# Kernel optimization log

Measured on AMD Instinct MI355X. Metric: run time of the kernel, lower is better.

## Reference

```python
import math
import jax, jax.numpy as jnp
import numpy as np

D_MODEL = 1024
NHEAD = 16
DK = D_MODEL // NHEAD
FACTOR = 5
B, L = 4, 8192
U = max(1, min(FACTOR * math.ceil(math.log(L + 1)), L))  # 50


def setup_inputs() -> dict:
    key = jax.random.key(0)
    ks = jax.random.split(key, 10)
    s = 1.0 / math.sqrt(D_MODEL)
    inp = {
        "x": jax.random.normal(ks[0], (B, L, D_MODEL), dtype=jnp.float32),
        "Wq": jax.random.normal(ks[1], (D_MODEL, D_MODEL), dtype=jnp.float32) * s,
        "bq": jnp.zeros((D_MODEL,), dtype=jnp.float32),
        "Wk": jax.random.normal(ks[2], (D_MODEL, D_MODEL), dtype=jnp.float32) * s,
        "bk": jnp.zeros((D_MODEL,), dtype=jnp.float32),
        "Wv": jax.random.normal(ks[3], (D_MODEL, D_MODEL), dtype=jnp.float32) * s,
        "bv": jnp.zeros((D_MODEL,), dtype=jnp.float32),
        "Wo": jax.random.normal(ks[4], (D_MODEL, D_MODEL), dtype=jnp.float32) * s,
        "bo": jnp.zeros((D_MODEL,), dtype=jnp.float32),
        # randperm(L)[:U] sample of key positions (constant, like torch.randperm)
        "idx_k": jax.random.permutation(ks[5], L)[:U].astype(jnp.int32),
    }
    return inp


def reference(x, Wq, bq, Wk, bk, Wv, bv, Wo, bo, idx_k):
    Bv, Lv, _ = x.shape
    H, dk = NHEAD, DK
    u = idx_k.shape[0]
    scale = 1.0 / math.sqrt(dk)

    # projections -> [B, H, L, dk]
    Q = (x @ Wq.T + bq).reshape(Bv, Lv, H, dk).transpose(0, 2, 1, 3)
    K = (x @ Wk.T + bk).reshape(Bv, Lv, H, dk).transpose(0, 2, 1, 3)
    V = (x @ Wv.T + bv).reshape(Bv, Lv, H, dk).transpose(0, 2, 1, 3)

    # sampled scores against u random keys: [B, H, L, u]
    K_samp = K[:, :, idx_k, :]
    scores = jnp.einsum("bhld,bhud->bhlu", Q, K_samp) * scale
    M = scores.max(-1) - scores.mean(-1)                 # [B, H, L]
    _, top_idx = jax.lax.top_k(M, u)                      # [B, H, u]

    # gather selected queries and attend against ALL keys
    Q_top = jnp.take_along_axis(Q, top_idx[..., None], axis=2)   # [B, H, u, dk]
    attn = jax.nn.softmax(jnp.einsum("bhud,bhld->bhul", Q_top, K) * scale, axis=-1)
    ctx_top = jnp.einsum("bhul,bhld->bhud", attn, V)              # [B, H, u, dk]

    # mean(V) fallback, scatter selected contexts back
    ctx = jnp.broadcast_to(V.mean(axis=2, keepdims=True), (Bv, H, Lv, dk))
    bidx = jnp.arange(Bv)[:, None, None]
    hidx = jnp.arange(H)[None, :, None]
    ctx = ctx.at[bidx, hidx, top_idx].set(ctx_top)

    ctx = ctx.transpose(0, 2, 1, 3).reshape(Bv, Lv, H * dk)
    return ctx @ Wo.T + bo
```

## Files before the change

### kernel.cpp

```cpp
#include <hip/hip_runtime.h>
#include <hip/hip_bf16.h>

#define B_ 4
#define L_ 8192
#define D_ 1024
#define H_ 16
#define SCALE 0.125f
#define NC 8
#define QPAD 64
#define RS 72

typedef __attribute__((ext_vector_type(8))) short bf16x8;
typedef __attribute__((ext_vector_type(4))) float f32x4;

__device__ __forceinline__ void gl2lds16(const void* g, void* s) {
    __builtin_amdgcn_global_load_lds(
        (const __attribute__((address_space(1))) unsigned int*)g,
        (__attribute__((address_space(3))) unsigned int*)s, 16, 0, 0);
}

__device__ __forceinline__ unsigned short bfbits(float a) {
    __hip_bfloat16 h = __float2bfloat16(a);
    return *(unsigned short*)&h;
}
__device__ __forceinline__ float bf2f(unsigned short u) {
    return __uint_as_float(((unsigned)u) << 16);
}

__global__ __launch_bounds__(256) void split3_kernel(const float* __restrict__ in,
        unsigned short* __restrict__ ph, unsigned short* __restrict__ pm,
        unsigned short* __restrict__ pl, int n4) {
    int i = blockIdx.x * 256 + threadIdx.x;
    if (i >= n4) return;
    float4 v = ((const float4*)in)[i];
    float c[4] = {v.x, v.y, v.z, v.w};
    unsigned short h[4], m[4], l[4];
    #pragma unroll
    for (int j = 0; j < 4; ++j) {
        float a = c[j];
        unsigned short hb = bfbits(a);
        float rh = a - bf2f(hb);
        unsigned short mb = bfbits(rh);
        float rm = rh - bf2f(mb);
        h[j] = hb; m[j] = mb; l[j] = bfbits(rm);
    }
    ((ushort4*)ph)[i] = *(ushort4*)h;
    ((ushort4*)pm)[i] = *(ushort4*)m;
    ((ushort4*)pl)[i] = *(ushort4*)l;
}

__global__ __launch_bounds__(256) void split2_kernel(const float* __restrict__ in,
        unsigned short* __restrict__ ph, unsigned short* __restrict__ pm, int n4) {
    int i = blockIdx.x * 256 + threadIdx.x;
    if (i >= n4) return;
    float4 v = ((const float4*)in)[i];
    float c[4] = {v.x, v.y, v.z, v.w};
    unsigned short h[4], m[4];
    #pragma unroll
    for (int j = 0; j < 4; ++j) {
        float a = c[j];
        unsigned short hb = bfbits(a);
        float rh = a - bf2f(hb);
        h[j] = hb; m[j] = bfbits(rh);
    }
    ((ushort4*)ph)[i] = *(ushort4*)h;
    ((ushort4*)pm)[i] = *(ushort4*)m;
}

__global__ __launch_bounds__(256) void xmean_kernel(const float* __restrict__ x,
                                                    float* __restrict__ xmean) {
    int c = blockIdx.x;
    int j = blockIdx.y * 256 + threadIdx.x;
    int b = blockIdx.z;
    const float* xp = x + ((size_t)b * L_ + (size_t)c * 256) * D_ + j;
    float s = 0.f;
    for (int l = 0; l < 256; ++l) s += xp[(size_t)l * D_];
    atomicAdd(&xmean[b * D_ + j], s * (1.0f / L_));
}

__global__ __launch_bounds__(256) void vecmat_kernel(const float* __restrict__ in,
                                                     const float* __restrict__ W,
                                                     const float* __restrict__ bias,
                                                     float* __restrict__ out) {
    __shared__ float vs[D_];
    int b = blockIdx.y;
    int j = blockIdx.x * 256 + threadIdx.x;
    for (int t = threadIdx.x; t < D_; t += 256) vs[t] = in[b * D_ + t];
    __syncthreads();
    const float* wr = W + (size_t)j * D_;
    float acc = 0.f;
    #pragma unroll 4
    for (int k = 0; k < D_; k += 4) {
        float4 w4 = *(const float4*)(wr + k);
        acc += vs[k] * w4.x + vs[k + 1] * w4.y + vs[k + 2] * w4.z + vs[k + 3] * w4.w;
    }
    out[b * D_ + j] = acc + bias[j];
}

__global__ __launch_bounds__(256) void ksamp_kernel(const float* __restrict__ x,
                                                    const float* __restrict__ Wk,
                                                    const float* __restrict__ bk,
                                                    const int* __restrict__ idx_k,
                                                    float* __restrict__ Ksamp, int U) {
    __shared__ float vs[D_];
    int u = blockIdx.x, b = blockIdx.y;
    int row = idx_k[u];
    const float* xp = x + ((size_t)b * L_ + row) * D_;
    for (int t = threadIdx.x; t < D_; t += 256) vs[t] = xp[t];
    __syncthreads();
    #pragma unroll
    for (int r = 0; r < 4; ++r) {
        int j = r * 256 + threadIdx.x;
        const float* wr = Wk + (size_t)j * D_;
        float acc = 0.f;
        #pragma unroll 4
        for (int k = 0; k < D_; k += 4) {
            float4 w4 = *(const float4*)(wr + k);
            acc += vs[k] * w4.x + vs[k + 1] * w4.y + vs[k + 2] * w4.z + vs[k + 3] * w4.w;
        }
        Ksamp[((size_t)b * U + u) * D_ + j] = acc + bk[j];
    }
}

#define TM 128
#define TN 128
#define BK 32
#define TSZ (TM * BK)

__global__ __launch_bounds__(256) void qkv_mfma(
    const unsigned short* __restrict__ xh, const unsigned short* __restrict__ xm,
    const unsigned short* __restrict__ xl,
    const unsigned short* __restrict__ qh, const unsigned short* __restrict__ qm,
    const unsigned short* __restrict__ ql,
    const unsigned short* __restrict__ kh, const unsigned short* __restrict__ km,
    const unsigned short* __restrict__ vh, const unsigned short* __restrict__ vm,
    const float* __restrict__ bq, const float* __restrict__ bk2, const float* __restrict__ bv,
    float* __restrict__ Q, __hip_bfloat16* __restrict__ Kb, __hip_bfloat16* __restrict__ Vb) {
    __shared__ __align__(16) unsigned short As[3][TSZ];
    __shared__ __align__(16) unsigned short Bs[3][TSZ];

    const int f    = blockIdx.y * 24 + blockIdx.x;
    const int w    = (f & 7) * 768 + (f >> 3);
    const int mblk = w / 24;
    const int nblk = w - mblk * 24;
    const int m0   = mblk * TM;
    const int n0   = nblk * TN;
    const int tid  = threadIdx.x;

    const float* bias; int which; int nb;
    if (n0 < 1024)      { which = 0; nb = n0;        bias = bq;  }
    else if (n0 < 2048) { which = 1; nb = n0 - 1024; bias = bk2; }
    else                { which = 2; nb = n0 - 2048; bias = bv;  }

    const int srow = tid >> 2;
    const int scol = (tid & 3) * 8;

    const int wave = tid >> 6;
    const int lane = tid & 63;
    const int wm = (wave & 1) * 64;
    const int wn = (wave >> 1) * 64;
    const int fr = lane & 15;
    const int fk = (lane >> 4) * 8;
    const int rbase = (lane >> 4) * 4;

    f32x4 acc[4][4];
    #pragma unroll
    for (int i = 0; i < 4; ++i)
        #pragma unroll
        for (int j = 0; j < 4; ++j)
            acc[i][j] = (f32x4){0.f, 0.f, 0.f, 0.f};

    const size_t aBase = (size_t)(m0 + srow) * D_ + scol;
    const size_t bBase = (size_t)(nb + srow) * D_ + scol;

    bf16x8 af[4], bfv[4];
    auto loadA = [&](const unsigned short* t) {
        #pragma unroll
        for (int i = 0; i < 4; ++i)
            af[i] = *(const bf16x8*)(t + (wm + i * 16 + fr) * BK + fk);
    };
    auto loadB = [&](const unsigned short* t) {
        #pragma unroll
        for (int j = 0; j < 4; ++j)
            bfv[j] = *(const bf16x8*)(t + (wn + j * 16 + fr) * BK + fk);
    };
    auto prod = [&]() {
        #pragma unroll
        for (int i = 0; i < 4; ++i)
            #pragma unroll
            for (int j = 0; j < 4; ++j)
                acc[i][j] = __builtin_amdgcn_mfma_f32_16x16x32_bf16(
                    af[i], bfv[j], acc[i][j], 0, 0, 0);
    };
    auto stage = [&](const unsigned short* g, unsigned short* s, int kt, size_t base) {
        gl2lds16(g + base + kt, s + tid * 8);
        gl2lds16(g + base + (size_t)64 * D_ + kt, s + tid * 8 + 2048);
    };

    if (which == 0) {
        for (int kt = 0; kt < D_; kt += BK) {
            stage(xh, &As[0][0], kt, aBase);
            stage(xm, &As[1][0], kt, aBase);
            stage(xl, &As[2][0], kt, aBase);
            stage(qh, &Bs[0][0], kt, bBase);
            stage(qm, &Bs[1][0], kt, bBase);
            stage(ql, &Bs[2][0], kt, bBase);
            __syncthreads();
            loadA(&As[0][0]); loadB(&Bs[0][0]); prod();
            loadB(&Bs[1][0]); prod();
            loadB(&Bs[2][0]); prod();
            loadA(&As[1][0]); loadB(&Bs[0][0]); prod();
            loadB(&Bs[1][0]); prod();
            loadA(&As[2][0]); loadB(&Bs[0][0]); prod();
            __syncthreads();
        }
    } else {
        const unsigned short* Bh = (which == 1) ? kh : vh;
        const unsigned short* Bm = (which == 1) ? km : vm;
        for (int kt = 0; kt < D_; kt += BK) {
            stage(xh, &As[0][0], kt, aBase);
            stage(xm, &As[1][0], kt, aBase);
            stage(Bh, &Bs[0][0], kt, bBase);
            stage(Bm, &Bs[1][0], kt, bBase);
            __syncthreads();
            loadA(&As[0][0]); loadB(&Bs[0][0]); prod();
            loadB(&Bs[1][0]); prod();
            loadA(&As[1][0]); loadB(&Bs[0][0]); prod();
            __syncthreads();
        }
    }

    float biasv[4];
    #pragma unroll
    for (int j = 0; j < 4; ++j) biasv[j] = bias[nb + wn + j * 16 + fr];

    #pragma unroll
    for (int i = 0; i < 4; ++i) {
        #pragma unroll
        for (int r = 0; r < 4; ++r) {
            size_t row = (size_t)(m0 + wm + i * 16 + rbase + r);
            #pragma unroll
            for (int j = 0; j < 4; ++j) {
                float v = acc[i][j][r] + biasv[j];
                int n = nb + wn + j * 16 + fr;
                if (which == 0)      Q[row * D_ + n] = v;
                else if (which == 1) Kb[row * D_ + n] = __float2bfloat16(v);
                else                 Vb[row * D_ + n] = __float2bfloat16(v);
            }
        }
    }
}

__global__ __launch_bounds__(256) void m_kernel(const float* __restrict__ Q,
                                                const float* __restrict__ Ksamp,
                                                float* __restrict__ M, int U) {
    __shared__ float ks[64 * 64];
    int lc = blockIdx.x, h = blockIdx.y, b = blockIdx.z;
    for (int t = threadIdx.x; t < U * 64; t += 256) {
        int u = t >> 6, d = t & 63;
        ks[t] = Ksamp[((size_t)b * U + u) * D_ + h * 64 + d];
    }
    __syncthreads();
    int l = lc * 256 + threadIdx.x;
    const float* qp = Q + ((size_t)b * L_ + l) * D_ + h * 64;
    float q[64];
    #pragma unroll
    for (int i = 0; i < 16; ++i) *(float4*)&q[i * 4] = *(const float4*)(qp + i * 4);
    float mx = -INFINITY, sm = 0.f;
    for (int u = 0; u < U; ++u) {
        const float* kp = &ks[u * 64];
        float dot = 0.f;
        #pragma unroll
        for (int d = 0; d < 64; ++d) dot = fmaf(q[d], kp[d], dot);
        dot *= SCALE;
        mx = fmaxf(mx, dot);
        sm += dot;
    }
    M[((size_t)(b * H_ + h)) * L_ + l] = mx - sm / (float)U;
}

__global__ __launch_bounds__(256) void topk_kernel(const float* __restrict__ M,
                                                   int* __restrict__ topidx, int U) {
    __shared__ float vals[L_];
    __shared__ float wv[4];
    __shared__ int   wi[4];
    __shared__ int   sbest;
    int bh = blockIdx.x;
    const float* mp = M + (size_t)bh * L_;
    for (int t = threadIdx.x; t < L_; t += 256) vals[t] = mp[t];
    __syncthreads();

    float bv = -INFINITY; int bi = 0x7fffffff;
    for (int t = threadIdx.x; t < L_; t += 256) {
        float v = vals[t];
        if (v > bv || (v == bv && t < bi)) { bv = v; bi = t; }
    }
    const int lane = threadIdx.x & 63, wave = threadIdx.x >> 6;

    for (int u = 0; u < U; ++u) {
        float rv = bv; int ri = bi;
        #pragma unroll
        for (int s = 1; s < 64; s <<= 1) {
            float v2 = __shfl_xor(rv, s, 64);
            int   i2 = __shfl_xor(ri, s, 64);
            if (v2 > rv || (v2 == rv && i2 < ri)) { rv = v2; ri = i2; }
        }
        if (lane == 0) { wv[wave] = rv; wi[wave] = ri; }
        __syncthreads();
        if (threadIdx.x == 0) {
            float fv = wv[0]; int fi = wi[0];
            #pragma unroll
            for (int w = 1; w < 4; ++w) {
                if (wv[w] > fv || (wv[w] == fv && wi[w] < fi)) { fv = wv[w]; fi = wi[w]; }
            }
            topidx[bh * U + u] = fi;
            sbest = fi;
            vals[fi] = -INFINITY;
        }
        __syncthreads();
        int fi = sbest;
        if ((fi & 255) == threadIdx.x) {
            bv = -INFINITY; bi = 0x7fffffff;
            for (int t = threadIdx.x; t < L_; t += 256) {
                float v = vals[t];
                if (v > bv || (v == bv && t < bi)) { bv = v; bi = t; }
            }
        }
    }
}

__global__ __launch_bounds__(256) void attn_mfma(const float* __restrict__ Q,
        const __hip_bfloat16* __restrict__ Kb, const __hip_bfloat16* __restrict__ Vb,
        const int* __restrict__ topidx,
        float* __restrict__ part_m, float* __restrict__ part_s,
        float* __restrict__ part_acc, int U) {
    __shared__ __align__(16) unsigned short Qh[QPAD * RS];
    __shared__ __align__(16) unsigned short Qm[QPAD * RS];
    __shared__ __align__(16) unsigned short Ks[64 * RS];
    __shared__ __align__(16) unsigned short Vt[64 * RS];
    __shared__ __align__(16) unsigned short Ph[QPAD * RS];

    const int c = blockIdx.x, h = blockIdx.y, b = blockIdx.z;
    const int bh = b * H_ + h;
    const int tid = threadIdx.x;
    const int wave = tid >> 6, lane = tid & 63;
    const int w16 = wave * 16;
    const int fr = lane & 15;
    const int quad = lane >> 4;
    const int fk = quad * 8;
    const int l0 = c * (L_ / NC);

    {
        int u = tid >> 2;
        int d0 = (tid & 3) * 16;
        unsigned short hbuf[16], mbuf[16];
        if (u < U) {
            int row = topidx[bh * U + u];
            const float* qp = Q + ((size_t)b * L_ + row) * D_ + h * 64 + d0;
            #pragma unroll
            for (int i = 0; i < 16; ++i) {
                float v = qp[i] * SCALE;
                unsigned short hb = bfbits(v);
                hbuf[i] = hb;
                mbuf[i] = bfbits(v - bf2f(hb));
            }
        } else {
            #pragma unroll
            for (int i = 0; i < 16; ++i) { hbuf[i] = 0; mbuf[i] = 0; }
        }
        #pragma unroll
        for (int i = 0; i < 2; ++i) {
            *(uint4*)&Qh[u * RS + d0 + i * 8] = ((uint4*)hbuf)[i];
            *(uint4*)&Qm[u * RS + d0 + i * 8] = ((uint4*)mbuf)[i];
        }
    }

    float m_r[4], s_r[4];
    f32x4 acc_o[4];
    #pragma unroll
    for (int r = 0; r < 4; ++r) { m_r[r] = -INFINITY; s_r[r] = 0.f; }
    #pragma unroll
    for (int n = 0; n < 4; ++n) acc_o[n] = (f32x4){0.f, 0.f, 0.f, 0.f};

    __syncthreads();

    for (int kt = 0; kt < L_ / NC; kt += 64) {
        {
            int key = tid >> 3;
            int d0 = (tid & 7) * 8;
            const __hip_bfloat16* kp = Kb + ((size_t)b * L_ + l0 + kt) * D_ + h * 64;
            *(uint4*)&Ks[key * RS + d0] = *(const uint4*)(kp + (size_t)key * D_ + d0);
            *(uint4*)&Ks[(key + 32) * RS + d0] =
                *(const uint4*)(kp + (size_t)(key + 32) * D_ + d0);
        }
        {
            int key = tid >> 2;
            int d0 = (tid & 3) * 16;
            const __hip_bfloat16* vp =
                Vb + ((size_t)b * L_ + l0 + kt + key) * D_ + h * 64 + d0;
            unsigned short vbuf[16];
            *(uint4*)&vbuf[0] = *(const uint4*)(vp);
            *(uint4*)&vbuf[8] = *(const uint4*)(vp + 8);
            #pragma unroll
            for (int i = 0; i < 16; ++i) Vt[(d0 + i) * RS + key] = vbuf[i];
        }
        __syncthreads();

        f32x4 sacc[4];
        #pragma unroll
        for (int n = 0; n < 4; ++n) {
            sacc[n] = (f32x4){0.f, 0.f, 0.f, 0.f};
            #pragma unroll
            for (int ks = 0; ks < 2; ++ks) {
                int k0 = ks * 32;
                bf16x8 ah = *(const bf16x8*)&Qh[(w16 + fr) * RS + k0 + fk];
                bf16x8 am = *(const bf16x8*)&Qm[(w16 + fr) * RS + k0 + fk];
                bf16x8 bb = *(const bf16x8*)&Ks[(n * 16 + fr) * RS + k0 + fk];
                sacc[n] = __builtin_amdgcn_mfma_f32_16x16x32_bf16(ah, bb, sacc[n], 0, 0, 0);
                sacc[n] = __builtin_amdgcn_mfma_f32_16x16x32_bf16(am, bb, sacc[n], 0, 0, 0);
            }
        }

        float p[4][4];
        #pragma unroll
        for (int r = 0; r < 4; ++r) {
            float rowmax = fmaxf(fmaxf(sacc[0][r], sacc[1][r]),
                                 fmaxf(sacc[2][r], sacc[3][r]));
            #pragma unroll
            for (int msk = 1; msk <= 8; msk <<= 1)
                rowmax = fmaxf(rowmax, __shfl_xor(rowmax, msk, 64));
            float mnew = fmaxf(m_r[r], rowmax);
            float alpha = __expf(m_r[r] - mnew);
            float rowsum = 0.f;
            #pragma unroll
            for (int n = 0; n < 4; ++n) {
                p[n][r] = __expf(sacc[n][r] - mnew);
                rowsum += p[n][r];
            }
            #pragma unroll
            for (int msk = 1; msk <= 8; msk <<= 1)
                rowsum += __shfl_xor(rowsum, msk, 64);
            s_r[r] = s_r[r] * alpha + rowsum;
            m_r[r] = mnew;
            #pragma unroll
            for (int n = 0; n < 4; ++n) acc_o[n][r] *= alpha;
        }

        #pragma unroll
        for (int r = 0; r < 4; ++r)
            #pragma unroll
            for (int n = 0; n < 4; ++n)
                Ph[(w16 + quad * 4 + r) * RS + n * 16 + fr] = bfbits(p[n][r]);

        #pragma unroll
        for (int n = 0; n < 4; ++n) {
            #pragma unroll
            for (int ks = 0; ks < 2; ++ks) {
                int k0 = ks * 32;
                bf16x8 pa = *(const bf16x8*)&Ph[(w16 + fr) * RS + k0 + fk];
                bf16x8 vb = *(const bf16x8*)&Vt[(n * 16 + fr) * RS + k0 + fk];
                acc_o[n] = __builtin_amdgcn_mfma_f32_16x16x32_bf16(pa, vb, acc_o[n], 0, 0, 0);
            }
        }
        __syncthreads();
    }

    #pragma unroll
    for (int r = 0; r < 4; ++r) {
        int q = w16 + quad * 4 + r;
        if (q < U) {
            size_t base = ((size_t)(bh * QPAD + q)) * NC + c;
            if (fr == 0) { part_m[base] = m_r[r]; part_s[base] = s_r[r]; }
            #pragma unroll
            for (int n = 0; n < 4; ++n)
                part_acc[base * 64 + n * 16 + fr] = acc_o[n][r];
        }
    }
}

__global__ __launch_bounds__(64) void attn_combine(const float* __restrict__ part_m,
        const float* __restrict__ part_s, const float* __restrict__ part_acc,
        float* __restrict__ ctx_top, int U) {
    int u = blockIdx.x, h = blockIdx.y, b = blockIdx.z;
    int bh = b * H_ + h;
    int d = threadIdx.x;
    size_t base = ((size_t)(bh * QPAD + u)) * NC;
    float M = -INFINITY;
    #pragma unroll
    for (int c = 0; c < NC; ++c) M = fmaxf(M, part_m[base + c]);
    float S = 0.f, A = 0.f;
    #pragma unroll
    for (int c = 0; c < NC; ++c) {
        float f = __expf(part_m[base + c] - M);
        S += part_s[base + c] * f;
        A += part_acc[(base + c) * 64 + d] * f;
    }
    ctx_top[(((size_t)bh) * U + u) * 64 + d] = A / S;
}

__global__ __launch_bounds__(256) void fill_base_kernel(const float* __restrict__ base,
                                                        float* __restrict__ out) {
    size_t i = (size_t)blockIdx.x * 256 + threadIdx.x;
    int col4 = (int)(i & 255);
    int b = (int)(i >> 21);
    ((float4*)out)[i] = ((const float4*)base)[b * 256 + col4];
}

__global__ __launch_bounds__(256) void delta_kernel(const float* __restrict__ ctx_top,
        const float* __restrict__ vmean, const float* __restrict__ Wo,
        const int* __restrict__ topidx, float* __restrict__ out, int U) {
    __shared__ float cd[64];
    int u = blockIdx.x, h = blockIdx.y, b = blockIdx.z;
    int row = topidx[(b * H_ + h) * U + u];
    if (threadIdx.x < 64) {
        cd[threadIdx.x] = ctx_top[(((size_t)(b * H_ + h)) * U + u) * 64 + threadIdx.x]
                        - vmean[b * D_ + h * 64 + threadIdx.x];
    }
    __syncthreads();
    float* op = out + ((size_t)b * L_ + row) * D_;
    #pragma unroll
    for (int r = 0; r < 4; ++r) {
        int j = r * 256 + threadIdx.x;
        const float* wr = Wo + (size_t)j * D_ + h * 64;
        float dlt = 0.f;
        #pragma unroll
        for (int k = 0; k < 64; k += 4) {
            float4 w4 = *(const float4*)(wr + k);
            dlt += cd[k] * w4.x + cd[k + 1] * w4.y + cd[k + 2] * w4.z + cd[k + 3] * w4.w;
        }
        atomicAdd(op + j, dlt);
    }
}

extern "C" void kernel_launch(void* const* d_in, const int* in_sizes, int n_in,
                              void* d_out, int out_size, void* d_ws, size_t ws_size,
                              hipStream_t stream) {
    const float* x   = (const float*)d_in[0];
    const float* Wq  = (const float*)d_in[1];
    const float* bq  = (const float*)d_in[2];
    const float* Wk  = (const float*)d_in[3];
    const float* bk  = (const float*)d_in[4];
    const float* Wv  = (const float*)d_in[5];
    const float* bv  = (const float*)d_in[6];
    const float* Wo  = (const float*)d_in[7];
    const float* bo  = (const float*)d_in[8];
    const int* idx_k = (const int*)d_in[9];
    const int U = in_sizes[9];
    float* out = (float*)d_out;
    (void)n_in; (void)ws_size;

    char* ws = (char*)d_ws;
    size_t off = 0;
    auto alloc = [&](size_t bytes) -> void* {
        void* p = ws + off;
        off += (bytes + 255) & ~(size_t)255;
        return p;
    };
    float* Q              = (float*)alloc((size_t)B_ * L_ * D_ * 4);
    __hip_bfloat16* Kb    = (__hip_bfloat16*)alloc((size_t)B_ * L_ * D_ * 2);
    __hip_bfloat16* Vb    = (__hip_bfloat16*)alloc((size_t)B_ * L_ * D_ * 2);
    unsigned short* xh    = (unsigned short*)alloc((size_t)B_ * L_ * D_ * 2);
    unsigned short* xm    = (unsigned short*)alloc((size_t)B_ * L_ * D_ * 2);
    unsigned short* xl    = (unsigned short*)alloc((size_t)B_ * L_ * D_ * 2);
    unsigned short* wqh   = (unsigned short*)alloc((size_t)D_ * D_ * 2);
    unsigned short* wqm   = (unsigned short*)alloc((size_t)D_ * D_ * 2);
    unsigned short* wql   = (unsigned short*)alloc((size_t)D_ * D_ * 2);
    unsigned short* wkh   = (unsigned short*)alloc((size_t)D_ * D_ * 2);
    unsigned short* wkm   = (unsigned short*)alloc((size_t)D_ * D_ * 2);
    unsigned short* wvh   = (unsigned short*)alloc((size_t)D_ * D_ * 2);
    unsigned short* wvm   = (unsigned short*)alloc((size_t)D_ * D_ * 2);
    float* Ksamp          = (float*)alloc((size_t)B_ * 64 * D_ * 4);
    float* Mbuf           = (float*)alloc((size_t)B_ * H_ * L_ * 4);
    int*   topidx         = (int*)alloc((size_t)B_ * H_ * 64 * 4);
    float* xmean          = (float*)alloc((size_t)B_ * D_ * 4);
    float* vmean          = (float*)alloc((size_t)B_ * D_ * 4);
    float* base           = (float*)alloc((size_t)B_ * D_ * 4);
    float* ctxt           = (float*)alloc((size_t)B_ * H_ * 64 * 64 * 4);
    float* part_m         = (float*)alloc((size_t)B_ * H_ * QPAD * NC * 4);
    float* part_s         = (float*)alloc((size_t)B_ * H_ * QPAD * NC * 4);
    float* part_acc       = (float*)alloc((size_t)B_ * H_ * QPAD * NC * 64 * 4);

    hipMemsetAsync(xmean, 0, (size_t)B_ * D_ * 4, stream);
    xmean_kernel<<<dim3(32, 4, B_), 256, 0, stream>>>(x, xmean);
    vecmat_kernel<<<dim3(4, B_), 256, 0, stream>>>(xmean, Wv, bv, vmean);
    vecmat_kernel<<<dim3(4, B_), 256, 0, stream>>>(vmean, Wo, bo, base);
    ksamp_kernel<<<dim3(U, B_), 256, 0, stream>>>(x, Wk, bk, idx_k, Ksamp, U);

    const int n4x = B_ * L_ * D_ / 4;
    const int n4w = D_ * D_ / 4;
    split3_kernel<<<dim3(n4x / 256), 256, 0, stream>>>(x, xh, xm, xl, n4x);
    split3_kernel<<<dim3(n4w / 256), 256, 0, stream>>>(Wq, wqh, wqm, wql, n4w);
    split2_kernel<<<dim3(n4w / 256), 256, 0, stream>>>(Wk, wkh, wkm, n4w);
    split2_kernel<<<dim3(n4w / 256), 256, 0, stream>>>(Wv, wvh, wvm, n4w);

    qkv_mfma<<<dim3(24, 256), 256, 0, stream>>>(xh, xm, xl, wqh, wqm, wql,
                                                wkh, wkm, wvh, wvm,
                                                bq, bk, bv, Q, Kb, Vb);

    m_kernel<<<dim3(32, H_, B_), 256, 0, stream>>>(Q, Ksamp, Mbuf, U);
    topk_kernel<<<dim3(B_ * H_), 256, 0, stream>>>(Mbuf, topidx, U);
    attn_mfma<<<dim3(NC, H_, B_), 256, 0, stream>>>(Q, Kb, Vb, topidx,
                                                    part_m, part_s, part_acc, U);
    attn_combine<<<dim3(U, H_, B_), 64, 0, stream>>>(part_m, part_s, part_acc, ctxt, U);
    fill_base_kernel<<<dim3(out_size / 4 / 256), 256, 0, stream>>>(base, out);
    delta_kernel<<<dim3(U, H_, B_), 256, 0, stream>>>(ctxt, vmean, Wo, topidx, out, U);
}
```

Before: 1.805 ms.

## Prefetch K/V tiles into registers, add MFMA priority hints, simplify QKV block mapping

The attention partial kernel now loads the next K/V tile from global memory into registers while the current tile's MFMAs run, then writes it to LDS between two barriers, overlapping global latency with compute. s_setprio raises wave priority around the MFMA sections. Separately, the QKV GEMM drops its swizzled block-index remapping in favor of plain blockIdx.x/y tiling, which may reduce L2 locality. The prefetch costs extra registers and an additional barrier per iteration.

```diff
diff --git a/kernel.cpp b/kernel.cpp
--- a/kernel.cpp
+++ b/kernel.cpp
@@ -139,13 +139,9 @@
     __shared__ __align__(16) unsigned short As[3][TSZ];
     __shared__ __align__(16) unsigned short Bs[3][TSZ];
 
-    const int f    = blockIdx.y * 24 + blockIdx.x;
-    const int w    = (f & 7) * 768 + (f >> 3);
-    const int mblk = w / 24;
-    const int nblk = w - mblk * 24;
-    const int m0   = mblk * TM;
-    const int n0   = nblk * TN;
-    const int tid  = threadIdx.x;
+    const int n0 = blockIdx.x * TN;
+    const int m0 = blockIdx.y * TM;
+    const int tid = threadIdx.x;
 
     const float* bias; int which; int nb;
     if (n0 < 1024)      { which = 0; nb = n0;        bias = bq;  }
@@ -375,6 +371,30 @@
         }
     }
 
+    const int kkey = tid >> 3, kd0 = (tid & 7) * 8;
+    const int vkey = tid >> 2, vd0 = (tid & 3) * 16;
+    const __hip_bfloat16* kbase = Kb + ((size_t)b * L_ + l0) * D_ + h * 64;
+    const __hip_bfloat16* vbase = Vb + ((size_t)b * L_ + l0) * D_ + h * 64;
+
+    uint4 kr0, kr1, vr0, vr1;
+    auto loadKV = [&](int t) {
+        const __hip_bfloat16* kp = kbase + (size_t)t * 64 * D_;
+        const __hip_bfloat16* vp = vbase + (size_t)t * 64 * D_ + (size_t)vkey * D_ + vd0;
+        kr0 = *(const uint4*)(kp + (size_t)kkey * D_ + kd0);
+        kr1 = *(const uint4*)(kp + (size_t)(kkey + 32) * D_ + kd0);
+        vr0 = *(const uint4*)(vp);
+        vr1 = *(const uint4*)(vp + 8);
+    };
+    auto writeKV = [&]() {
+        *(uint4*)&Ks[kkey * RS + kd0] = kr0;
+        *(uint4*)&Ks[(kkey + 32) * RS + kd0] = kr1;
+        unsigned short vb_[16];
+        *(uint4*)&vb_[0] = vr0;
+        *(uint4*)&vb_[8] = vr1;
+        #pragma unroll
+        for (int i = 0; i < 16; ++i) Vt[(vd0 + i) * RS + vkey] = vb_[i];
+    };
+
     float m_r[4], s_r[4];
     f32x4 acc_o[4];
     #pragma unroll
@@ -382,31 +402,16 @@
     #pragma unroll
     for (int n = 0; n < 4; ++n) acc_o[n] = (f32x4){0.f, 0.f, 0.f, 0.f};
 
+    loadKV(0);
+    writeKV();
     __syncthreads();
 
-    for (int kt = 0; kt < L_ / NC; kt += 64) {
-        {
-            int key = tid >> 3;
-            int d0 = (tid & 7) * 8;
-            const __hip_bfloat16* kp = Kb + ((size_t)b * L_ + l0 + kt) * D_ + h * 64;
-            *(uint4*)&Ks[key * RS + d0] = *(const uint4*)(kp + (size_t)key * D_ + d0);
-            *(uint4*)&Ks[(key + 32) * RS + d0] =
-                *(const uint4*)(kp + (size_t)(key + 32) * D_ + d0);
-        }
-        {
-            int key = tid >> 2;
-            int d0 = (tid & 3) * 16;
-            const __hip_bfloat16* vp =
-                Vb + ((size_t)b * L_ + l0 + kt + key) * D_ + h * 64 + d0;
-            unsigned short vbuf[16];
-            *(uint4*)&vbuf[0] = *(const uint4*)(vp);
-            *(uint4*)&vbuf[8] = *(const uint4*)(vp + 8);
-            #pragma unroll
-            for (int i = 0; i < 16; ++i) Vt[(d0 + i) * RS + key] = vbuf[i];
-        }
-        __syncthreads();
+    const int NT = (L_ / NC) / 64;
+    for (int t = 0; t < NT; ++t) {
+        if (t + 1 < NT) loadKV(t + 1);
 
         f32x4 sacc[4];
+        __builtin_amdgcn_s_setprio(1);
         #pragma unroll
         for (int n = 0; n < 4; ++n) {
             sacc[n] = (f32x4){0.f, 0.f, 0.f, 0.f};
@@ -420,6 +425,7 @@
                 sacc[n] = __builtin_amdgcn_mfma_f32_16x16x32_bf16(am, bb, sacc[n], 0, 0, 0);
             }
         }
+        __builtin_amdgcn_s_setprio(0);
 
         float p[4][4];
         #pragma unroll
@@ -452,6 +458,7 @@
             for (int n = 0; n < 4; ++n)
                 Ph[(w16 + quad * 4 + r) * RS + n * 16 + fr] = bfbits(p[n][r]);
 
+        __builtin_amdgcn_s_setprio(1);
         #pragma unroll
         for (int n = 0; n < 4; ++n) {
             #pragma unroll
@@ -462,7 +469,13 @@
                 acc_o[n] = __builtin_amdgcn_mfma_f32_16x16x32_bf16(pa, vb, acc_o[n], 0, 0, 0);
             }
         }
-        __syncthreads();
+        __builtin_amdgcn_s_setprio(0);
+
+        if (t + 1 < NT) {
+            __syncthreads();
+            writeKV();
+            __syncthreads();
+        }
     }
 
     #pragma unroll
```

Measured after the change: 1.770 ms. Within noise of the previous version (-1.9%).
